# Kernel tuning notes

Hardware: AMD Instinct MI355X
Metric: run time of the kernel (lower is better)

The kernel has to match this reference:

```python
import jax, jax.numpy as jnp
import numpy as np

EPS = 1e-6
NUM_HEADS = 8
NUM_TOKENS = 196

def setup_inputs() -> dict:
    key = jax.random.key(0)
    ks = jax.random.split(key, 4)
    B, N, C = 32, 3136, 384
    H, Dh, M = NUM_HEADS, C // NUM_HEADS, NUM_TOKENS
    return {
        "x": jax.random.normal(ks[0], (B, N, C), dtype=jnp.float32),
        "q_param": jax.random.normal(ks[1], (1, M, H, Dh), dtype=jnp.float32) * 0.02,
        "kv_w": jax.random.normal(ks[2], (2 * C, C), dtype=jnp.float32) * 0.02,
        "proj_w": jax.random.normal(ks[3], (C, C), dtype=jnp.float32) * 0.02,
        "proj_b": jnp.zeros((C,), dtype=jnp.float32),
        "ln_w": jnp.ones((C,), dtype=jnp.float32),
        "ln_b": jnp.zeros((C,), dtype=jnp.float32),
    }

def reference(x, q_param, kv_w, proj_w, proj_b, ln_w, ln_b):
    B, N, C = x.shape
    H = NUM_HEADS
    Dh = C // H
    # LayerNorm (eps=1e-6)
    mu = jnp.mean(x, axis=-1, keepdims=True)
    var = jnp.mean(jnp.square(x - mu), axis=-1, keepdims=True)
    x = (x - mu) * jax.lax.rsqrt(var + EPS) * ln_w + ln_b
    # exact GELU (nn.GELU default)
    x = jax.nn.gelu(x, approximate=False)
    # kv projection (no bias): [B,N,2C] -> k,v each [B,H,N,Dh]
    kv = (x @ kv_w.T).reshape(B, N, 2, H, Dh)
    kv = jnp.transpose(kv, (2, 0, 3, 1, 4))
    k, v = kv[0], kv[1]
    # learnable queries: (1,M,H,Dh) -> (1,H,M,Dh)
    q = jnp.transpose(q_param, (0, 2, 1, 3))
    # NOTE: source applies NO 1/sqrt(Dh) scaling
    attn = jnp.einsum("bhmd,bhnd->bhmn", jnp.broadcast_to(q, (B, H, NUM_TOKENS, Dh)), k)
    attn = jax.nn.softmax(attn, axis=-1)
    out = jnp.einsum("bhmn,bhnd->bhmd", attn, v)  # [B,H,M,Dh]
    out = jnp.transpose(out, (0, 2, 1, 3)).reshape(B, NUM_TOKENS, C)
    return out @ proj_w.T + proj_b
```

## Files before the change

### kernel.cpp

```cpp
#include <hip/hip_runtime.h>
#include <stdint.h>

typedef float f32x4 __attribute__((ext_vector_type(4)));
typedef short s16x8 __attribute__((ext_vector_type(8)));
typedef short s16x4 __attribute__((ext_vector_type(4)));
typedef unsigned short ushort_t;

#define B_  32
#define N_  3136
#define C_  384
#define H_  8
#define DH_ 48
#define M_  196
#define ROWS  (B_*N_)
#define PROWS (B_*M_)

static __device__ __forceinline__ ushort_t f2bf(float f) {
  union { float f; uint32_t u; } v; v.f = f;
  uint32_t r = (v.u + 0x7fffu + ((v.u >> 16) & 1u)) >> 16;
  return (ushort_t)r;
}

static __device__ __forceinline__ f32x4 mfma_16x16x32(s16x8 a, s16x8 b, f32x4 c) {
  return __builtin_amdgcn_mfma_f32_16x16x32_bf16(a, b, c, 0, 0, 0);
}

static __device__ __forceinline__ f32x4 mfma_16x16x16(s16x4 a, s16x4 b, f32x4 c) {
#if __has_builtin(__builtin_amdgcn_mfma_f32_16x16x16_bf16)
  return __builtin_amdgcn_mfma_f32_16x16x16_bf16(a, b, c, 0, 0, 0);
#elif __has_builtin(__builtin_amdgcn_mfma_f32_16x16x16bf16_1k)
  return __builtin_amdgcn_mfma_f32_16x16x16bf16_1k(a, b, c, 0, 0, 0);
#else
  f32x4 d;
  asm("v_mfma_f32_16x16x16_bf16 %0, %1, %2, %3" : "=v"(d) : "v"(a), "v"(b), "v"(c));
  return d;
#endif
}

static __device__ __forceinline__ void gload_lds16(const void* g, void* l) {
  __builtin_amdgcn_global_load_lds(
      (const __attribute__((address_space(1))) void*)(uintptr_t)g,
      (__attribute__((address_space(3))) void*)(uint32_t)(uintptr_t)l,
      16, 0, 0);
}

__global__ __launch_bounds__(256) void k_ln_gelu(
    const float* __restrict__ x, const float* __restrict__ lnw,
    const float* __restrict__ lnb, ushort_t* __restrict__ x16) {
  int row = blockIdx.x * 4 + (threadIdx.x >> 6);
  int lane = threadIdx.x & 63;
  const float2* xr = (const float2*)(x + (size_t)row * C_);
  float2 v0 = xr[lane], v1 = xr[lane + 64], v2 = xr[lane + 128];
  float s  = v0.x + v0.y + v1.x + v1.y + v2.x + v2.y;
  float ss = v0.x*v0.x + v0.y*v0.y + v1.x*v1.x + v1.y*v1.y + v2.x*v2.x + v2.y*v2.y;
#pragma unroll
  for (int off = 1; off < 64; off <<= 1) {
    s  += __shfl_xor(s, off);
    ss += __shfl_xor(ss, off);
  }
  float mu = s * (1.0f / C_);
  float rs = rsqrtf(ss * (1.0f / C_) - mu * mu + 1e-6f);
  const float2* wr = (const float2*)lnw;
  const float2* br = (const float2*)lnb;
  uint32_t* outp = (uint32_t*)(x16 + (size_t)row * C_);
#pragma unroll
  for (int t = 0; t < 3; ++t) {
    int idx = lane + t * 64;
    float2 v = (t == 0) ? v0 : ((t == 1) ? v1 : v2);
    float2 w = wr[idx], bb = br[idx];
    float a0 = (v.x - mu) * rs * w.x + bb.x;
    float a1 = (v.y - mu) * rs * w.y + bb.y;
    a0 = 0.5f * a0 * (1.0f + erff(a0 * 0.70710678118654752440f));
    a1 = 0.5f * a1 * (1.0f + erff(a1 * 0.70710678118654752440f));
    outp[idx] = (uint32_t)f2bf(a0) | ((uint32_t)f2bf(a1) << 16);
  }
}

__global__ __launch_bounds__(256) void k_convert(
    const float* __restrict__ kvw, const float* __restrict__ pw,
    const float* __restrict__ qp, ushort_t* __restrict__ wkv16,
    ushort_t* __restrict__ wp16, ushort_t* __restrict__ q16) {
  int i = blockIdx.x * 256 + threadIdx.x;
  if (i < 2 * C_ * C_) wkv16[i] = f2bf(kvw[i]);
  if (i < C_ * C_)     wp16[i]  = f2bf(pw[i]);
  if (i < M_ * H_ * DH_) {
    int d = i % DH_; int t = i / DH_; int h = t % H_; int m = t / H_;
    q16[((size_t)h * M_ + m) * DH_ + d] = f2bf(qp[i]);
  }
}

template <typename OutT, bool BIAS>
__global__ __launch_bounds__(256) void k_gemm_bt(
    const ushort_t* __restrict__ A, const ushort_t* __restrict__ Bw,
    OutT* __restrict__ Co, const float* __restrict__ bias,
    int M, int N, int K, int ntn) {
  __shared__ ushort_t lA[128 * 32];
  __shared__ ushort_t lB[128 * 32];
  int tr = blockIdx.x / ntn, tc = blockIdx.x % ntn;
  int tid = threadIdx.x;
  int w = tid >> 6, l = tid & 63;
  int wr = w >> 1, wc = w & 1;
  int c = l & 15, g = l >> 4;
  f32x4 acc[4][4];
#pragma unroll
  for (int i = 0; i < 4; ++i)
#pragma unroll
    for (int j = 0; j < 4; ++j) acc[i][j] = (f32x4){0.f, 0.f, 0.f, 0.f};
  const size_t a0 = (size_t)tr * 128, b0 = (size_t)tc * 128;
  int srow = l >> 2;
  int scol = (l & 3) * 8;
  for (int kt = 0; kt < K; kt += 32) {
    __syncthreads();
#pragma unroll
    for (int r = 0; r < 2; ++r) {
      int lr = w * 16 + r * 64;
      gload_lds16(A  + (a0 + lr + srow) * (size_t)K + kt + scol, &lA[lr * 32]);
      gload_lds16(Bw + (b0 + lr + srow) * (size_t)K + kt + scol, &lB[lr * 32]);
    }
    __syncthreads();
    s16x8 af[4], bf[4];
#pragma unroll
    for (int i = 0; i < 4; ++i)
      af[i] = *(const s16x8*)&lA[(wr * 64 + i * 16 + c) * 32 + g * 8];
#pragma unroll
    for (int j = 0; j < 4; ++j)
      bf[j] = *(const s16x8*)&lB[(wc * 64 + j * 16 + c) * 32 + g * 8];
#pragma unroll
    for (int i = 0; i < 4; ++i)
#pragma unroll
      for (int j = 0; j < 4; ++j)
        acc[i][j] = mfma_16x16x32(af[i], bf[j], acc[i][j]);
  }
#pragma unroll
  for (int i = 0; i < 4; ++i) {
#pragma unroll
    for (int j = 0; j < 4; ++j) {
      size_t col = b0 + wc * 64 + j * 16 + c;
      float bs = BIAS ? bias[col] : 0.0f;
#pragma unroll
      for (int q = 0; q < 4; ++q) {
        size_t row = a0 + wr * 64 + i * 16 + g * 4 + q;
        float v = acc[i][j][q] + bs;
        if constexpr (sizeof(OutT) == 2) Co[row * N + col] = f2bf(v);
        else                             Co[row * N + col] = v;
      }
    }
  }
}

__global__ __launch_bounds__(512) void k_attn(
    const ushort_t* __restrict__ kv, const ushort_t* __restrict__ q16,
    ushort_t* __restrict__ att16) {
  int b = blockIdx.x >> 3, h = blockIdx.x & 7;
  __shared__ ushort_t Kl[64 * 72];
  __shared__ ushort_t Vt[48 * 72];
  int tid = threadIdx.x;
  int w = tid >> 6, l = tid & 63;
  int c = l & 15, g = l >> 4;
  for (int i = tid; i < 64 * 72; i += 512) Kl[i] = 0;
  for (int i = tid; i < 48 * 72; i += 512) Vt[i] = 0;
  s16x8 qf[2][2];
#pragma unroll
  for (int i = 0; i < 2; ++i)
#pragma unroll
    for (int kk = 0; kk < 2; ++kk) {
      int m = w * 32 + i * 16 + c;
      int dh = kk * 32 + g * 8;
      s16x8 z = {0, 0, 0, 0, 0, 0, 0, 0};
      qf[i][kk] = (m < M_ && dh < DH_)
                      ? *(const s16x8*)(q16 + ((size_t)h * M_ + m) * DH_ + dh)
                      : z;
    }
  f32x4 o[3][2];
#pragma unroll
  for (int f = 0; f < 3; ++f)
#pragma unroll
    for (int i = 0; i < 2; ++i) o[f][i] = (f32x4){0.f, 0.f, 0.f, 0.f};
  float rm[2] = {-3e38f, -3e38f}, rl[2] = {0.f, 0.f};
  int srow = tid >> 3, spart = tid & 7;
  for (int t = 0; t < 49; ++t) {
    __syncthreads();
    size_t gb = ((size_t)b * N_ + t * 64 + srow) * (size_t)(2 * C_) + h * DH_ + spart * 6;
    uint32_t k0 = *(const uint32_t*)(kv + gb);
    uint32_t k1 = *(const uint32_t*)(kv + gb + 2);
    uint32_t k2 = *(const uint32_t*)(kv + gb + 4);
    uint32_t* kd = (uint32_t*)&Kl[srow * 72 + spart * 6];
    kd[0] = k0; kd[1] = k1; kd[2] = k2;
    uint32_t v0 = *(const uint32_t*)(kv + gb + C_);
    uint32_t v1 = *(const uint32_t*)(kv + gb + C_ + 2);
    uint32_t v2 = *(const uint32_t*)(kv + gb + C_ + 4);
    int dbase = spart * 6;
    Vt[(dbase + 0) * 72 + srow] = (ushort_t)v0;
    Vt[(dbase + 1) * 72 + srow] = (ushort_t)(v0 >> 16);
    Vt[(dbase + 2) * 72 + srow] = (ushort_t)v1;
    Vt[(dbase + 3) * 72 + srow] = (ushort_t)(v1 >> 16);
    Vt[(dbase + 4) * 72 + srow] = (ushort_t)v2;
    Vt[(dbase + 5) * 72 + srow] = (ushort_t)(v2 >> 16);
    __syncthreads();
    f32x4 s[4][2];
#pragma unroll
    for (int j = 0; j < 4; ++j) {
      s16x8 kf0 = *(const s16x8*)&Kl[(j * 16 + c) * 72 + g * 8];
      s16x8 kf1 = *(const s16x8*)&Kl[(j * 16 + c) * 72 + 32 + g * 8];
#pragma unroll
      for (int i = 0; i < 2; ++i) {
        f32x4 z = {0.f, 0.f, 0.f, 0.f};
        f32x4 t0 = mfma_16x16x32(kf0, qf[i][0], z);
        s[j][i] = mfma_16x16x32(kf1, qf[i][1], t0);
      }
    }
#pragma unroll
    for (int i = 0; i < 2; ++i) {
      float tm = s[0][i][0];
#pragma unroll
      for (int j = 0; j < 4; ++j)
#pragma unroll
        for (int q = 0; q < 4; ++q) tm = fmaxf(tm, s[j][i][q]);
      tm = fmaxf(tm, __shfl_xor(tm, 16));
      tm = fmaxf(tm, __shfl_xor(tm, 32));
      float nm = fmaxf(rm[i], tm);
      float corr = __expf(rm[i] - nm);
      rm[i] = nm;
      s16x4 pb[4];
      float ts = 0.f;
#pragma unroll
      for (int j = 0; j < 4; ++j) {
        float p0 = __expf(s[j][i][0] - nm);
        float p1 = __expf(s[j][i][1] - nm);
        float p2 = __expf(s[j][i][2] - nm);
        float p3 = __expf(s[j][i][3] - nm);
        ts += p0 + p1 + p2 + p3;
        pb[j] = (s16x4){(short)f2bf(p0), (short)f2bf(p1),
                        (short)f2bf(p2), (short)f2bf(p3)};
      }
      ts += __shfl_xor(ts, 16);
      ts += __shfl_xor(ts, 32);
      rl[i] = rl[i] * corr + ts;
#pragma unroll
      for (int f = 0; f < 3; ++f) {
        o[f][i] *= corr;
#pragma unroll
        for (int j = 0; j < 4; ++j) {
          s16x4 vf = *(const s16x4*)&Vt[(f * 16 + c) * 72 + j * 16 + g * 4];
          o[f][i] = mfma_16x16x16(vf, pb[j], o[f][i]);
        }
      }
    }
  }
#pragma unroll
  for (int i = 0; i < 2; ++i) {
    int m = w * 32 + i * 16 + c;
    if (m < M_) {
      float inv = 1.0f / rl[i];
#pragma unroll
      for (int f = 0; f < 3; ++f)
#pragma unroll
        for (int q = 0; q < 4; ++q) {
          int d = f * 16 + g * 4 + q;
          att16[((size_t)b * M_ + m) * C_ + h * DH_ + d] = f2bf(o[f][i][q] * inv);
        }
    }
  }
}

extern "C" void kernel_launch(void* const* d_in, const int* in_sizes, int n_in,
                              void* d_out, int out_size, void* d_ws, size_t ws_size,
                              hipStream_t stream) {
  (void)in_sizes; (void)n_in; (void)out_size; (void)ws_size;
  const float* x   = (const float*)d_in[0];
  const float* qp  = (const float*)d_in[1];
  const float* kvw = (const float*)d_in[2];
  const float* pw  = (const float*)d_in[3];
  const float* pbv = (const float*)d_in[4];
  const float* lnw = (const float*)d_in[5];
  const float* lnb = (const float*)d_in[6];
  float* out = (float*)d_out;

  ushort_t* x16   = (ushort_t*)d_ws;
  ushort_t* kv16  = x16 + (size_t)ROWS * C_;
  ushort_t* att16 = kv16 + (size_t)ROWS * 2 * C_;
  ushort_t* wkv16 = att16 + (size_t)PROWS * C_;
  ushort_t* wp16  = wkv16 + 2 * C_ * C_;
  ushort_t* q16   = wp16 + C_ * C_;

  hipLaunchKernelGGL(k_ln_gelu, dim3(ROWS / 4), dim3(256), 0, stream, x, lnw, lnb, x16);
  hipLaunchKernelGGL(k_convert, dim3((2 * C_ * C_ + 255) / 256), dim3(256), 0, stream,
                     kvw, pw, qp, wkv16, wp16, q16);
  hipLaunchKernelGGL((k_gemm_bt<ushort_t, false>),
                     dim3((ROWS / 128) * (2 * C_ / 128)), dim3(256), 0, stream,
                     x16, wkv16, kv16, (const float*)nullptr, ROWS, 2 * C_, C_, 2 * C_ / 128);
  hipLaunchKernelGGL(k_attn, dim3(B_ * H_), dim3(512), 0, stream, kv16, q16, att16);
  hipLaunchKernelGGL((k_gemm_bt<float, true>),
                     dim3((PROWS / 128) * (C_ / 128)), dim3(256), 0, stream,
                     att16, wp16, out, pbv, PROWS, C_, C_, C_ / 128);
}
```

Measured before the change: 303.1 us.

## Prefetch next KV tile into registers and pad V transpose buffer in attention

```diff
diff --git a/kernel.cpp b/kernel.cpp
--- a/kernel.cpp
+++ b/kernel.cpp
@@ -153,12 +153,12 @@
     ushort_t* __restrict__ att16) {
   int b = blockIdx.x >> 3, h = blockIdx.x & 7;
   __shared__ ushort_t Kl[64 * 72];
-  __shared__ ushort_t Vt[48 * 72];
+  __shared__ ushort_t Vt[48 * 76];
   int tid = threadIdx.x;
   int w = tid >> 6, l = tid & 63;
   int c = l & 15, g = l >> 4;
   for (int i = tid; i < 64 * 72; i += 512) Kl[i] = 0;
-  for (int i = tid; i < 48 * 72; i += 512) Vt[i] = 0;
+  for (int i = tid; i < 48 * 76; i += 512) Vt[i] = 0;
   s16x8 qf[2][2];
 #pragma unroll
   for (int i = 0; i < 2; ++i)
@@ -178,25 +178,40 @@
     for (int i = 0; i < 2; ++i) o[f][i] = (f32x4){0.f, 0.f, 0.f, 0.f};
   float rm[2] = {-3e38f, -3e38f}, rl[2] = {0.f, 0.f};
   int srow = tid >> 3, spart = tid & 7;
+  const size_t rowstride = (size_t)(2 * C_);
+  uint32_t kr0, kr1, kr2, vr0, vr1, vr2;
+  {
+    size_t gb = ((size_t)b * N_ + srow) * rowstride + h * DH_ + spart * 6;
+    kr0 = *(const uint32_t*)(kv + gb);
+    kr1 = *(const uint32_t*)(kv + gb + 2);
+    kr2 = *(const uint32_t*)(kv + gb + 4);
+    vr0 = *(const uint32_t*)(kv + gb + C_);
+    vr1 = *(const uint32_t*)(kv + gb + C_ + 2);
+    vr2 = *(const uint32_t*)(kv + gb + C_ + 4);
+  }
+  __syncthreads();
+
   for (int t = 0; t < 49; ++t) {
+    uint32_t* kd = (uint32_t*)&Kl[srow * 72 + spart * 6];
+    kd[0] = kr0; kd[1] = kr1; kd[2] = kr2;
+    int dbase = spart * 6;
+    Vt[(dbase + 0) * 76 + srow] = (ushort_t)vr0;
+    Vt[(dbase + 1) * 76 + srow] = (ushort_t)(vr0 >> 16);
+    Vt[(dbase + 2) * 76 + srow] = (ushort_t)vr1;
+    Vt[(dbase + 3) * 76 + srow] = (ushort_t)(vr1 >> 16);
+    Vt[(dbase + 4) * 76 + srow] = (ushort_t)vr2;
+    Vt[(dbase + 5) * 76 + srow] = (ushort_t)(vr2 >> 16);
     __syncthreads();
-    size_t gb = ((size_t)b * N_ + t * 64 + srow) * (size_t)(2 * C_) + h * DH_ + spart * 6;
-    uint32_t k0 = *(const uint32_t*)(kv + gb);
-    uint32_t k1 = *(const uint32_t*)(kv + gb + 2);
-    uint32_t k2 = *(const uint32_t*)(kv + gb + 4);
-    uint32_t* kd = (uint32_t*)&Kl[srow * 72 + spart * 6];
-    kd[0] = k0; kd[1] = k1; kd[2] = k2;
-    uint32_t v0 = *(const uint32_t*)(kv + gb + C_);
-    uint32_t v1 = *(const uint32_t*)(kv + gb + C_ + 2);
-    uint32_t v2 = *(const uint32_t*)(kv + gb + C_ + 4);
-    int dbase = spart * 6;
-    Vt[(dbase + 0) * 72 + srow] = (ushort_t)v0;
-    Vt[(dbase + 1) * 72 + srow] = (ushort_t)(v0 >> 16);
-    Vt[(dbase + 2) * 72 + srow] = (ushort_t)v1;
-    Vt[(dbase + 3) * 72 + srow] = (ushort_t)(v1 >> 16);
-    Vt[(dbase + 4) * 72 + srow] = (ushort_t)v2;
-    Vt[(dbase + 5) * 72 + srow] = (ushort_t)(v2 >> 16);
-    __syncthreads();
+    {
+      int tn = (t < 48) ? t + 1 : t;
+      size_t gb = ((size_t)b * N_ + tn * 64 + srow) * rowstride + h * DH_ + spart * 6;
+      kr0 = *(const uint32_t*)(kv + gb);
+      kr1 = *(const uint32_t*)(kv + gb + 2);
+      kr2 = *(const uint32_t*)(kv + gb + 4);
+      vr0 = *(const uint32_t*)(kv + gb + C_);
+      vr1 = *(const uint32_t*)(kv + gb + C_ + 2);
+      vr2 = *(const uint32_t*)(kv + gb + C_ + 4);
+    }
     f32x4 s[4][2];
 #pragma unroll
     for (int j = 0; j < 4; ++j) {
@@ -209,6 +224,7 @@
         s[j][i] = mfma_16x16x32(kf1, qf[i][1], t0);
       }
     }
+    s16x4 pb[2][4];
 #pragma unroll
     for (int i = 0; i < 2; ++i) {
       float tm = s[0][i][0];
@@ -221,7 +237,6 @@
       float nm = fmaxf(rm[i], tm);
       float corr = __expf(rm[i] - nm);
       rm[i] = nm;
-      s16x4 pb[4];
       float ts = 0.f;
 #pragma unroll
       for (int j = 0; j < 4; ++j) {
@@ -229,23 +244,25 @@
         float p1 = __expf(s[j][i][1] - nm);
         float p2 = __expf(s[j][i][2] - nm);
         float p3 = __expf(s[j][i][3] - nm);
-        ts += p0 + p1 + p2 + p3;
-        pb[j] = (s16x4){(short)f2bf(p0), (short)f2bf(p1),
-                        (short)f2bf(p2), (short)f2bf(p3)};
+        ts += (p0 + p1) + (p2 + p3);
+        pb[i][j] = (s16x4){(short)f2bf(p0), (short)f2bf(p1),
+                           (short)f2bf(p2), (short)f2bf(p3)};
       }
       ts += __shfl_xor(ts, 16);
       ts += __shfl_xor(ts, 32);
       rl[i] = rl[i] * corr + ts;
 #pragma unroll
-      for (int f = 0; f < 3; ++f) {
-        o[f][i] *= corr;
-#pragma unroll
-        for (int j = 0; j < 4; ++j) {
-          s16x4 vf = *(const s16x4*)&Vt[(f * 16 + c) * 72 + j * 16 + g * 4];
-          o[f][i] = mfma_16x16x16(vf, pb[j], o[f][i]);
-        }
-      }
-    }
+      for (int f = 0; f < 3; ++f) o[f][i] *= corr;
+    }
+#pragma unroll
+    for (int f = 0; f < 3; ++f)
+#pragma unroll
+      for (int j = 0; j < 4; ++j) {
+        s16x4 vf = *(const s16x4*)&Vt[(f * 16 + c) * 76 + j * 16 + g * 4];
+        o[f][0] = mfma_16x16x16(vf, pb[0][j], o[f][0]);
+        o[f][1] = mfma_16x16x16(vf, pb[1][j], o[f][1]);
+      }
+    __syncthreads();
   }
 #pragma unroll
   for (int i = 0; i < 2; ++i) {
@@ -253,12 +270,14 @@
     if (m < M_) {
       float inv = 1.0f / rl[i];
 #pragma unroll
-      for (int f = 0; f < 3; ++f)
-#pragma unroll
-        for (int q = 0; q < 4; ++q) {
-          int d = f * 16 + g * 4 + q;
-          att16[((size_t)b * M_ + m) * C_ + h * DH_ + d] = f2bf(o[f][i][q] * inv);
-        }
+      for (int f = 0; f < 3; ++f) {
+        uint32_t w0 = (uint32_t)f2bf(o[f][i][0] * inv) |
+                      ((uint32_t)f2bf(o[f][i][1] * inv) << 16);
+        uint32_t w1 = (uint32_t)f2bf(o[f][i][2] * inv) |
+                      ((uint32_t)f2bf(o[f][i][3] * inv) << 16);
+        uint2 val; val.x = w0; val.y = w1;
+        *(uint2*)&att16[((size_t)b * M_ + m) * C_ + h * DH_ + f * 16 + g * 4] = val;
+      }
     }
   }
 }
```

Result: faster. 272.9 us (-10.0%).
